# Performance work log

Measured on AMD Instinct MI355X. Metric: run time of the kernel, lower is better.

Reference implementation:

```python
import jax, jax.numpy as jnp
import numpy as np

MOMENTUM = 0.9
BN_EPS = 1e-5
NORM_EPS = 1e-12
NUM_CLASSES = 10000
DIM_MLP = 512
NUM_EXPERTS = 3
FEAT_DIM = 256
N = 4096


def _l2norm(x, axis=-1):
    # F.normalize: x / max(||x||, eps)
    n = jnp.sqrt(jnp.sum(x * x, axis=axis, keepdims=True))
    return x / jnp.maximum(n, NORM_EPS)


def setup_inputs() -> dict:
    key = jax.random.key(0)
    ks = jax.random.split(key, 8)
    feat_in = jax.random.normal(ks[0], (N, DIM_MLP * NUM_EXPERTS), dtype=jnp.float32)
    label = jax.random.randint(ks[1], (N,), 0, NUM_CLASSES, dtype=jnp.int32)
    # encoder params
    W1 = jax.random.normal(ks[2], (DIM_MLP * NUM_EXPERTS, DIM_MLP), dtype=jnp.float32) / np.sqrt(DIM_MLP * NUM_EXPERTS)
    b1 = jnp.zeros((DIM_MLP,), dtype=jnp.float32)
    gamma = jnp.ones((DIM_MLP,), dtype=jnp.float32)
    beta = jnp.zeros((DIM_MLP,), dtype=jnp.float32)
    W2 = jax.random.normal(ks[3], (DIM_MLP, FEAT_DIM), dtype=jnp.float32) / np.sqrt(DIM_MLP)
    b2 = jnp.zeros((FEAT_DIM,), dtype=jnp.float32)
    # memory bank buffer: randn then row-normalized (as in __init__)
    memory_pt = _l2norm(jax.random.normal(ks[4], (NUM_CLASSES, FEAT_DIM), dtype=jnp.float32))
    return {"feat_in": feat_in, "label": label, "W1": W1, "b1": b1,
            "gamma": gamma, "beta": beta, "W2": W2, "b2": b2,
            "memory_pt": memory_pt}


def _encoder(feat_in, W1, b1, gamma, beta, W2, b2):
    h = feat_in @ W1 + b1                       # [N, dim_mlp]
    # BatchNorm1d in training mode: batch statistics (biased variance)
    mu = jnp.mean(h, axis=0)
    var = jnp.mean((h - mu) ** 2, axis=0)
    h = (h - mu) * jax.lax.rsqrt(var + BN_EPS) * gamma + beta
    h = jax.nn.relu(h)
    out = h @ W2 + b2                           # [N, 256]
    return _l2norm(out, axis=1)


def _update_memory(memory_pt, feat, label):
    # Strictly sequential per-sample momentum update (order matters for
    # duplicate labels), each touched row renormalized — lax.scan recurrence.
    def step(mem, xy):
        x, y = xy
        pt = MOMENTUM * mem[y] + (1.0 - MOMENTUM) * x
        pt = _l2norm(pt, axis=0)
        return mem.at[y].set(pt), None
    mem, _ = jax.lax.scan(step, memory_pt, (feat, label))
    return mem


def reference(feat_in, label, W1, b1, gamma, beta, W2, b2, memory_pt):
    feat = _encoder(feat_in, W1, b1, gamma, beta, W2, b2)   # [N, 256], unit rows
    # memory_pt.detach(): no grad flows through the memory bank
    mem = _update_memory(jax.lax.stop_gradient(memory_pt),
                         jax.lax.stop_gradient(feat), label)
    mem = jax.lax.stop_gradient(mem)
    sim_logit = jnp.einsum('nc,kc->nk', feat, mem)          # [N, K]
    return sim_logit
```

## Files before the change

kernel.cpp:

```cpp
#include <hip/hip_runtime.h>
#include <stdint.h>

typedef _Float16 f16;
typedef _Float16 f16x2 __attribute__((ext_vector_type(2)));
typedef _Float16 f16x4 __attribute__((ext_vector_type(4)));
typedef _Float16 f16x8 __attribute__((ext_vector_type(8)));
typedef float f32x4 __attribute__((ext_vector_type(4)));

typedef __attribute__((address_space(1))) void gvoid;
typedef __attribute__((address_space(3))) void lvoid;

#define NROWS 4096
#define DIMIN 1536
#define DMLP 512
#define FDIM 256
#define NCLS 10000
#define NPAD 10112

__device__ __forceinline__ void load_lds16(const void* g, void* l) {
    __builtin_amdgcn_global_load_lds((gvoid*)g, (lvoid*)l, 16, 0, 0);
}

template<int TM, int TN>
__global__ __launch_bounds__(256) void gemm_t(
    const f16* __restrict__ A, const f16* __restrict__ Bt,
    float* __restrict__ C, const float* __restrict__ bias,
    int K, int ldc, int Nstore)
{
    constexpr int BK = 64;
    constexpr int AM = TM / 32;
    constexpr int AN = TN / 32;
    constexpr int CA = TM * 8;
    constexpr int CB = TN * 8;
    constexpr int RTOT = (CA + CB) / 256;

    __shared__ f16 As[TM * BK];
    __shared__ f16 Bs[TN * BK];

    const int tid  = threadIdx.x;
    const int lane = tid & 63;
    const int w    = tid >> 6;
    const int wm   = (w >> 1) * (TM / 2);
    const int wn   = (w & 1) * (TN / 2);
    const int row0 = blockIdx.x * TM;
    const int col0 = blockIdx.y * TN;
    const int quad = lane >> 4;
    const int r16  = lane & 15;

    f32x4 acc[AM][AN] = {};

    const f16* gsrc[RTOT];
    f16* ldst[RTOT];
#pragma unroll
    for (int r = 0; r < RTOT; ++r) {
        int c = tid + r * 256;
        bool isA = (c < CA);
        int cc = isA ? c : c - CA;
        int row = cc >> 3;
        int gs = (cc & 7) ^ (row & 7);
        gsrc[r] = (isA ? A + (size_t)(row0 + row) * K
                       : Bt + (size_t)(col0 + row) * K) + gs * 8;
        ldst[r] = (isA ? As : Bs) + cc * 8;
    }

    for (int k0 = 0; k0 < K; k0 += BK) {
#pragma unroll
        for (int r = 0; r < RTOT; ++r)
            load_lds16(gsrc[r] + k0, ldst[r]);
        __syncthreads();

#pragma unroll
        for (int ks = 0; ks < 2; ++ks) {
            f16x8 af[AM], bq[AN];
#pragma unroll
            for (int mi = 0; mi < AM; ++mi) {
                int row = wm + mi * 16 + r16;
                int slot = (ks * 4 + quad) ^ (r16 & 7);
                af[mi] = *(const f16x8*)&As[row * BK + slot * 8];
            }
#pragma unroll
            for (int ni = 0; ni < AN; ++ni) {
                int row = wn + ni * 16 + r16;
                int slot = (ks * 4 + quad) ^ (r16 & 7);
                bq[ni] = *(const f16x8*)&Bs[row * BK + slot * 8];
            }
#pragma unroll
            for (int mi = 0; mi < AM; ++mi)
#pragma unroll
                for (int ni = 0; ni < AN; ++ni)
                    acc[mi][ni] = __builtin_amdgcn_mfma_f32_16x16x32_f16(
                        af[mi], bq[ni], acc[mi][ni], 0, 0, 0);
        }
        __syncthreads();
    }

#pragma unroll
    for (int mi = 0; mi < AM; ++mi) {
#pragma unroll
        for (int ni = 0; ni < AN; ++ni) {
            int col = col0 + wn + ni * 16 + r16;
            if (col < Nstore) {
                float bv = bias ? bias[col] : 0.0f;
                int rowb = row0 + wm + mi * 16 + quad * 4;
#pragma unroll
                for (int r = 0; r < 4; ++r)
                    C[(size_t)(rowb + r) * ldc + col] = acc[mi][ni][r] + bv;
            }
        }
    }
}

__global__ void zero_k(float* __restrict__ p, int n) {
    int i = blockIdx.x * 256 + threadIdx.x;
    if (i < n) p[i] = 0.0f;
}

__global__ void f32_to_f16_k(const float* __restrict__ in, f16* __restrict__ out, int n4) {
    int i = blockIdx.x * 256 + threadIdx.x;
    if (i >= n4) return;
    float4 v = *(const float4*)&in[(size_t)i * 4];
    f16x4 o = {(f16)v.x, (f16)v.y, (f16)v.z, (f16)v.w};
    *(f16x4*)&out[(size_t)i * 4] = o;
}

__global__ void transpose_to_f16_k(const float* __restrict__ in, f16* __restrict__ out, int R, int C) {
    int idx = blockIdx.x * 256 + threadIdx.x;
    if (idx >= R * C) return;
    int n = idx / R, k = idx - n * R;
    out[idx] = (f16)in[(size_t)k * C + n];
}

__global__ void bn_stats_k(const float* __restrict__ h, float* __restrict__ sums, float* __restrict__ sqs) {
    int t = threadIdx.x, b = blockIdx.x;
    int c = t * 2;
    float s0 = 0.f, s1 = 0.f, q0 = 0.f, q1 = 0.f;
    for (int r = b; r < NROWS; r += 128) {
        float2 v = *(const float2*)&h[(size_t)r * DMLP + c];
        s0 += v.x; s1 += v.y; q0 += v.x * v.x; q1 += v.y * v.y;
    }
    atomicAdd(&sums[c], s0);
    atomicAdd(&sums[c + 1], s1);
    atomicAdd(&sqs[c], q0);
    atomicAdd(&sqs[c + 1], q1);
}

__global__ void bn_finish_k(const float* __restrict__ sums, const float* __restrict__ sqs,
                            const float* __restrict__ gamma, const float* __restrict__ beta,
                            float* __restrict__ scale, float* __restrict__ shift) {
    int c = blockIdx.x * 256 + threadIdx.x;
    if (c >= DMLP) return;
    const float inv_n = 1.0f / 4096.0f;
    float mu = sums[c] * inv_n;
    float var = fmaxf(sqs[c] * inv_n - mu * mu, 0.0f);
    float a = rsqrtf(var + 1e-5f) * gamma[c];
    scale[c] = a;
    shift[c] = beta[c] - mu * a;
}

__global__ void bn_apply_k(const float* __restrict__ h, const float* __restrict__ scale,
                           const float* __restrict__ shift, f16* __restrict__ out) {
    int i = blockIdx.x * 256 + threadIdx.x;
    int c = (i & 127) * 4;
    float4 v = *(const float4*)&h[(size_t)i * 4];
    float4 sc = *(const float4*)&scale[c];
    float4 sh = *(const float4*)&shift[c];
    f16x4 o = {(f16)fmaxf(v.x * sc.x + sh.x, 0.0f),
               (f16)fmaxf(v.y * sc.y + sh.y, 0.0f),
               (f16)fmaxf(v.z * sc.z + sh.z, 0.0f),
               (f16)fmaxf(v.w * sc.w + sh.w, 0.0f)};
    *(f16x4*)&out[(size_t)i * 4] = o;
}

__global__ void l2norm_k(const float* __restrict__ X, float* __restrict__ Y, f16* __restrict__ Yh) {
    int wv = (blockIdx.x * 256 + threadIdx.x) >> 6;
    int lane = threadIdx.x & 63;
    float4 v = *(const float4*)&X[(size_t)wv * FDIM + lane * 4];
    float s = v.x * v.x + v.y * v.y + v.z * v.z + v.w * v.w;
#pragma unroll
    for (int off = 32; off > 0; off >>= 1) s += __shfl_xor(s, off);
    float inv = 1.0f / fmaxf(sqrtf(s), 1e-12f);
    float4 o = {v.x * inv, v.y * inv, v.z * inv, v.w * inv};
    *(float4*)&Y[(size_t)wv * FDIM + lane * 4] = o;
    f16x4 oh = {(f16)o.x, (f16)o.y, (f16)o.z, (f16)o.w};
    *(f16x4*)&Yh[(size_t)wv * FDIM + lane * 4] = oh;
}

__global__ void chain_k(const int* __restrict__ label, const float* __restrict__ feat,
                        const float* __restrict__ mp, f16* __restrict__ memh) {
    int y = (blockIdx.x * 256 + threadIdx.x) >> 6;
    int lane = threadIdx.x & 63;
    float4 m = {0.f, 0.f, 0.f, 0.f};
    if (y < NCLS) {
        m = *(const float4*)&mp[(size_t)y * FDIM + lane * 4];
        for (int g = 0; g < 64; ++g) {
            int lab = label[g * 64 + lane];
            unsigned long long mask = __ballot(lab == y);
            while (mask) {
                int b = __builtin_ctzll(mask);
                mask &= mask - 1;
                int i = g * 64 + b;
                float4 x = *(const float4*)&feat[(size_t)i * FDIM + lane * 4];
                m.x = 0.9f * m.x + 0.1f * x.x;
                m.y = 0.9f * m.y + 0.1f * x.y;
                m.z = 0.9f * m.z + 0.1f * x.z;
                m.w = 0.9f * m.w + 0.1f * x.w;
                float s = m.x * m.x + m.y * m.y + m.z * m.z + m.w * m.w;
#pragma unroll
                for (int off = 32; off > 0; off >>= 1) s += __shfl_xor(s, off);
                float inv = 1.0f / fmaxf(sqrtf(s), 1e-12f);
                m.x *= inv; m.y *= inv; m.z *= inv; m.w *= inv;
            }
        }
    }
    f16x4 o = {(f16)m.x, (f16)m.y, (f16)m.z, (f16)m.w};
    *(f16x4*)&memh[(size_t)y * FDIM + lane * 4] = o;
}

extern "C" void kernel_launch(void* const* d_in, const int* in_sizes, int n_in,
                              void* d_out, int out_size, void* d_ws, size_t ws_size,
                              hipStream_t stream) {
    const float* feat_in = (const float*)d_in[0];
    const int*   label   = (const int*)d_in[1];
    const float* W1      = (const float*)d_in[2];
    const float* b1      = (const float*)d_in[3];
    const float* gamma   = (const float*)d_in[4];
    const float* beta    = (const float*)d_in[5];
    const float* W2      = (const float*)d_in[6];
    const float* b2      = (const float*)d_in[7];
    const float* mp      = (const float*)d_in[8];
    float* out = (float*)d_out;

    char* w = (char*)d_ws;
    f16* A1h   = (f16*)w;   w += (size_t)NROWS * DIMIN * 2;
    f16* W1t   = (f16*)w;   w += (size_t)DMLP * DIMIN * 2;
    f16* W2t   = (f16*)w;   w += (size_t)FDIM * DMLP * 2;
    float* h   = (float*)w; w += (size_t)NROWS * DMLP * 4;
    f16* h2    = (f16*)w;   w += (size_t)NROWS * DMLP * 2;
    float* out2= (float*)w; w += (size_t)NROWS * FDIM * 4;
    float* feat= (float*)w; w += (size_t)NROWS * FDIM * 4;
    f16* feath = (f16*)w;   w += (size_t)NROWS * FDIM * 2;
    f16* memh  = (f16*)w;   w += (size_t)NPAD * FDIM * 2;
    float* sums= (float*)w; w += DMLP * 4;
    float* sqs = (float*)w; w += DMLP * 4;
    float* bnsc= (float*)w; w += DMLP * 4;
    float* bnsh= (float*)w; w += DMLP * 4;

    zero_k<<<4, 256, 0, stream>>>(sums, 2 * DMLP);
    f32_to_f16_k<<<(NROWS * DIMIN / 4) / 256, 256, 0, stream>>>(feat_in, A1h, NROWS * DIMIN / 4);
    transpose_to_f16_k<<<(DIMIN * DMLP) / 256, 256, 0, stream>>>(W1, W1t, DIMIN, DMLP);
    transpose_to_f16_k<<<(DMLP * FDIM) / 256, 256, 0, stream>>>(W2, W2t, DMLP, FDIM);

    {
        dim3 g(NROWS / 64, DMLP / 64);
        gemm_t<64, 64><<<g, 256, 0, stream>>>(A1h, W1t, h, b1, DIMIN, DMLP, DMLP);
    }

    bn_stats_k<<<128, 256, 0, stream>>>(h, sums, sqs);
    bn_finish_k<<<2, 256, 0, stream>>>(sums, sqs, gamma, beta, bnsc, bnsh);
    bn_apply_k<<<(NROWS * DMLP / 4) / 256, 256, 0, stream>>>(h, bnsc, bnsh, h2);

    {
        dim3 g(NROWS / 64, FDIM / 64);
        gemm_t<64, 64><<<g, 256, 0, stream>>>(h2, W2t, out2, b2, DMLP, FDIM, FDIM);
    }

    l2norm_k<<<NROWS / 4, 256, 0, stream>>>(out2, feat, feath);

    chain_k<<<NPAD / 4, 256, 0, stream>>>(label, feat, mp, memh);

    {
        dim3 g(NROWS / 128, NPAD / 128);
        gemm_t<128, 128><<<g, 256, 0, stream>>>(feath, memh, out, nullptr, FDIM, NCLS, NCLS);
    }
}
```

Baseline: 322.8 us.

## Fuse prep kernels, BN finish into apply, L2 norm into second GEMM, retile final GEMM

Merges the zeroing, fp16 conversion and both weight transposes into one prep launch. Folds the BN finish step into the apply kernel. Adds a dedicated second GEMM with full-row tiles (32x256) that applies the bias and L2 normalization in its epilogue, which removes the intermediate buffer and the separate norm kernel. Changes the final similarity GEMM tile from 128x128 to 256x128. These cut launch count and intermediate memory traffic, at the cost of recomputing BN stats per thread and fewer blocks in the fused and retiled GEMMs.

```diff
diff --git a/kernel.cpp b/kernel.cpp
--- a/kernel.cpp
+++ b/kernel.cpp
@@ -71,19 +71,14 @@
 
 #pragma unroll
         for (int ks = 0; ks < 2; ++ks) {
+            const int slot = (ks * 4 + quad) ^ (r16 & 7);
             f16x8 af[AM], bq[AN];
 #pragma unroll
-            for (int mi = 0; mi < AM; ++mi) {
-                int row = wm + mi * 16 + r16;
-                int slot = (ks * 4 + quad) ^ (r16 & 7);
-                af[mi] = *(const f16x8*)&As[row * BK + slot * 8];
-            }
-#pragma unroll
-            for (int ni = 0; ni < AN; ++ni) {
-                int row = wn + ni * 16 + r16;
-                int slot = (ks * 4 + quad) ^ (r16 & 7);
-                bq[ni] = *(const f16x8*)&Bs[row * BK + slot * 8];
-            }
+            for (int mi = 0; mi < AM; ++mi)
+                af[mi] = *(const f16x8*)&As[(wm + mi * 16 + r16) * BK + slot * 8];
+#pragma unroll
+            for (int ni = 0; ni < AN; ++ni)
+                bq[ni] = *(const f16x8*)&Bs[(wn + ni * 16 + r16) * BK + slot * 8];
 #pragma unroll
             for (int mi = 0; mi < AM; ++mi)
 #pragma unroll
@@ -110,24 +105,127 @@
     }
 }
 
-__global__ void zero_k(float* __restrict__ p, int n) {
-    int i = blockIdx.x * 256 + threadIdx.x;
-    if (i < n) p[i] = 0.0f;
-}
-
-__global__ void f32_to_f16_k(const float* __restrict__ in, f16* __restrict__ out, int n4) {
-    int i = blockIdx.x * 256 + threadIdx.x;
-    if (i >= n4) return;
-    float4 v = *(const float4*)&in[(size_t)i * 4];
-    f16x4 o = {(f16)v.x, (f16)v.y, (f16)v.z, (f16)v.w};
-    *(f16x4*)&out[(size_t)i * 4] = o;
-}
-
-__global__ void transpose_to_f16_k(const float* __restrict__ in, f16* __restrict__ out, int R, int C) {
+__global__ __launch_bounds__(256) void gemm2_l2_k(
+    const f16* __restrict__ A, const f16* __restrict__ Bt,
+    const float* __restrict__ bias,
+    float* __restrict__ feat, f16* __restrict__ feath)
+{
+    constexpr int TM = 32, TN = 256, BK = 64, K = 512;
+    constexpr int AN = 8;
+    constexpr int CA = TM * 8;
+    constexpr int CB = TN * 8;
+    constexpr int RTOT = (CA + CB) / 256;
+
+    __shared__ f16 As[TM * BK];
+    __shared__ f16 Bs[TN * BK];
+    __shared__ float part[2][TM];
+
+    const int tid = threadIdx.x, lane = tid & 63, w = tid >> 6;
+    const int wm = (w >> 1) * 16;
+    const int wh = (w & 1);
+    const int wn = wh * 128;
+    const int row0 = blockIdx.x * TM;
+    const int quad = lane >> 4, r16 = lane & 15;
+
+    f32x4 acc[AN] = {};
+
+    const f16* gsrc[RTOT];
+    f16* ldst[RTOT];
+#pragma unroll
+    for (int r = 0; r < RTOT; ++r) {
+        int c = tid + r * 256;
+        bool isA = (c < CA);
+        int cc = isA ? c : c - CA;
+        int row = cc >> 3;
+        int gs = (cc & 7) ^ (row & 7);
+        gsrc[r] = (isA ? A + (size_t)(row0 + row) * K
+                       : Bt + (size_t)row * K) + gs * 8;
+        ldst[r] = (isA ? As : Bs) + cc * 8;
+    }
+
+    for (int k0 = 0; k0 < K; k0 += BK) {
+#pragma unroll
+        for (int r = 0; r < RTOT; ++r)
+            load_lds16(gsrc[r] + k0, ldst[r]);
+        __syncthreads();
+#pragma unroll
+        for (int ks = 0; ks < 2; ++ks) {
+            const int slot = (ks * 4 + quad) ^ (r16 & 7);
+            f16x8 af = *(const f16x8*)&As[(wm + r16) * BK + slot * 8];
+#pragma unroll
+            for (int ni = 0; ni < AN; ++ni) {
+                f16x8 bq = *(const f16x8*)&Bs[(wn + ni * 16 + r16) * BK + slot * 8];
+                acc[ni] = __builtin_amdgcn_mfma_f32_16x16x32_f16(af, bq, acc[ni], 0, 0, 0);
+            }
+        }
+        __syncthreads();
+    }
+
+    float s[4] = {0.f, 0.f, 0.f, 0.f};
+#pragma unroll
+    for (int ni = 0; ni < AN; ++ni) {
+        float b = bias[wn + ni * 16 + r16];
+#pragma unroll
+        for (int r = 0; r < 4; ++r) {
+            acc[ni][r] += b;
+            s[r] += acc[ni][r] * acc[ni][r];
+        }
+    }
+#pragma unroll
+    for (int off = 1; off < 16; off <<= 1)
+#pragma unroll
+        for (int r = 0; r < 4; ++r)
+            s[r] += __shfl_xor(s[r], off);
+    if (r16 == 0)
+#pragma unroll
+        for (int r = 0; r < 4; ++r)
+            part[wh][wm + quad * 4 + r] = s[r];
+    __syncthreads();
+
+    float inv[4];
+#pragma unroll
+    for (int r = 0; r < 4; ++r) {
+        int row = wm + quad * 4 + r;
+        float tot = part[0][row] + part[1][row];
+        inv[r] = 1.0f / fmaxf(sqrtf(tot), 1e-12f);
+    }
+#pragma unroll
+    for (int ni = 0; ni < AN; ++ni) {
+        int col = wn + ni * 16 + r16;
+#pragma unroll
+        for (int r = 0; r < 4; ++r) {
+            int row = row0 + wm + quad * 4 + r;
+            float v = acc[ni][r] * inv[r];
+            feat[(size_t)row * FDIM + col] = v;
+            feath[(size_t)row * FDIM + col] = (f16)v;
+        }
+    }
+}
+
+__global__ void prep_k(const float* __restrict__ feat_in, const float* __restrict__ W1,
+                       const float* __restrict__ W2, f16* __restrict__ A1h,
+                       f16* __restrict__ W1t, f16* __restrict__ W2t,
+                       float* __restrict__ stats) {
     int idx = blockIdx.x * 256 + threadIdx.x;
-    if (idx >= R * C) return;
-    int n = idx / R, k = idx - n * R;
-    out[idx] = (f16)in[(size_t)k * C + n];
+    if (idx < 1024) { stats[idx] = 0.0f; return; }
+    idx -= 1024;
+    if (idx < NROWS * DIMIN / 4) {
+        float4 v = *(const float4*)&feat_in[(size_t)idx * 4];
+        f16x4 o = {(f16)v.x, (f16)v.y, (f16)v.z, (f16)v.w};
+        *(f16x4*)&A1h[(size_t)idx * 4] = o;
+        return;
+    }
+    idx -= NROWS * DIMIN / 4;
+    if (idx < DMLP * DIMIN) {
+        int n = idx / DIMIN, k = idx - n * DIMIN;
+        W1t[idx] = (f16)W1[(size_t)k * DMLP + n];
+        return;
+    }
+    idx -= DMLP * DIMIN;
+    if (idx < FDIM * DMLP) {
+        int n = idx / DMLP, k = idx - n * DMLP;
+        W2t[idx] = (f16)W2[(size_t)k * FDIM + n];
+    }
 }
 
 __global__ void bn_stats_k(const float* __restrict__ h, float* __restrict__ sums, float* __restrict__ sqs) {
@@ -144,45 +242,28 @@
     atomicAdd(&sqs[c + 1], q1);
 }
 
-__global__ void bn_finish_k(const float* __restrict__ sums, const float* __restrict__ sqs,
-                            const float* __restrict__ gamma, const float* __restrict__ beta,
-                            float* __restrict__ scale, float* __restrict__ shift) {
-    int c = blockIdx.x * 256 + threadIdx.x;
-    if (c >= DMLP) return;
-    const float inv_n = 1.0f / 4096.0f;
-    float mu = sums[c] * inv_n;
-    float var = fmaxf(sqs[c] * inv_n - mu * mu, 0.0f);
-    float a = rsqrtf(var + 1e-5f) * gamma[c];
-    scale[c] = a;
-    shift[c] = beta[c] - mu * a;
-}
-
-__global__ void bn_apply_k(const float* __restrict__ h, const float* __restrict__ scale,
-                           const float* __restrict__ shift, f16* __restrict__ out) {
+__global__ void bn_apply_k(const float* __restrict__ h, const float* __restrict__ sums,
+                           const float* __restrict__ sqs, const float* __restrict__ gamma,
+                           const float* __restrict__ beta, f16* __restrict__ out) {
     int i = blockIdx.x * 256 + threadIdx.x;
     int c = (i & 127) * 4;
-    float4 v = *(const float4*)&h[(size_t)i * 4];
-    float4 sc = *(const float4*)&scale[c];
-    float4 sh = *(const float4*)&shift[c];
-    f16x4 o = {(f16)fmaxf(v.x * sc.x + sh.x, 0.0f),
-               (f16)fmaxf(v.y * sc.y + sh.y, 0.0f),
-               (f16)fmaxf(v.z * sc.z + sh.z, 0.0f),
-               (f16)fmaxf(v.w * sc.w + sh.w, 0.0f)};
+    float4 v  = *(const float4*)&h[(size_t)i * 4];
+    float4 sm = *(const float4*)&sums[c];
+    float4 sq = *(const float4*)&sqs[c];
+    float4 gm = *(const float4*)&gamma[c];
+    float4 bt = *(const float4*)&beta[c];
+    const float inv_n = 1.0f / 4096.0f;
+    float mu, var, a;
+    mu = sm.x * inv_n; var = fmaxf(sq.x * inv_n - mu * mu, 0.f); a = rsqrtf(var + 1e-5f) * gm.x;
+    float o0 = fmaxf((v.x - mu) * a + bt.x, 0.f);
+    mu = sm.y * inv_n; var = fmaxf(sq.y * inv_n - mu * mu, 0.f); a = rsqrtf(var + 1e-5f) * gm.y;
+    float o1 = fmaxf((v.y - mu) * a + bt.y, 0.f);
+    mu = sm.z * inv_n; var = fmaxf(sq.z * inv_n - mu * mu, 0.f); a = rsqrtf(var + 1e-5f) * gm.z;
+    float o2 = fmaxf((v.z - mu) * a + bt.z, 0.f);
+    mu = sm.w * inv_n; var = fmaxf(sq.w * inv_n - mu * mu, 0.f); a = rsqrtf(var + 1e-5f) * gm.w;
+    float o3 = fmaxf((v.w - mu) * a + bt.w, 0.f);
+    f16x4 o = {(f16)o0, (f16)o1, (f16)o2, (f16)o3};
     *(f16x4*)&out[(size_t)i * 4] = o;
-}
-
-__global__ void l2norm_k(const float* __restrict__ X, float* __restrict__ Y, f16* __restrict__ Yh) {
-    int wv = (blockIdx.x * 256 + threadIdx.x) >> 6;
-    int lane = threadIdx.x & 63;
-    float4 v = *(const float4*)&X[(size_t)wv * FDIM + lane * 4];
-    float s = v.x * v.x + v.y * v.y + v.z * v.z + v.w * v.w;
-#pragma unroll
-    for (int off = 32; off > 0; off >>= 1) s += __shfl_xor(s, off);
-    float inv = 1.0f / fmaxf(sqrtf(s), 1e-12f);
-    float4 o = {v.x * inv, v.y * inv, v.z * inv, v.w * inv};
-    *(float4*)&Y[(size_t)wv * FDIM + lane * 4] = o;
-    f16x4 oh = {(f16)o.x, (f16)o.y, (f16)o.z, (f16)o.w};
-    *(f16x4*)&Yh[(size_t)wv * FDIM + lane * 4] = oh;
 }
 
 __global__ void chain_k(const int* __restrict__ label, const float* __restrict__ feat,
@@ -236,19 +317,14 @@
     f16* W2t   = (f16*)w;   w += (size_t)FDIM * DMLP * 2;
     float* h   = (float*)w; w += (size_t)NROWS * DMLP * 4;
     f16* h2    = (f16*)w;   w += (size_t)NROWS * DMLP * 2;
-    float* out2= (float*)w; w += (size_t)NROWS * FDIM * 4;
     float* feat= (float*)w; w += (size_t)NROWS * FDIM * 4;
     f16* feath = (f16*)w;   w += (size_t)NROWS * FDIM * 2;
     f16* memh  = (f16*)w;   w += (size_t)NPAD * FDIM * 2;
     float* sums= (float*)w; w += DMLP * 4;
     float* sqs = (float*)w; w += DMLP * 4;
-    float* bnsc= (float*)w; w += DMLP * 4;
-    float* bnsh= (float*)w; w += DMLP * 4;
-
-    zero_k<<<4, 256, 0, stream>>>(sums, 2 * DMLP);
-    f32_to_f16_k<<<(NROWS * DIMIN / 4) / 256, 256, 0, stream>>>(feat_in, A1h, NROWS * DIMIN / 4);
-    transpose_to_f16_k<<<(DIMIN * DMLP) / 256, 256, 0, stream>>>(W1, W1t, DIMIN, DMLP);
-    transpose_to_f16_k<<<(DMLP * FDIM) / 256, 256, 0, stream>>>(W2, W2t, DMLP, FDIM);
+
+    prep_k<<<(1024 + NROWS * DIMIN / 4 + DMLP * DIMIN + FDIM * DMLP) / 256, 256, 0, stream>>>(
+        feat_in, W1, W2, A1h, W1t, W2t, sums);
 
     {
         dim3 g(NROWS / 64, DMLP / 64);
@@ -256,20 +332,15 @@
     }
 
     bn_stats_k<<<128, 256, 0, stream>>>(h, sums, sqs);
-    bn_finish_k<<<2, 256, 0, stream>>>(sums, sqs, gamma, beta, bnsc, bnsh);
-    bn_apply_k<<<(NROWS * DMLP / 4) / 256, 256, 0, stream>>>(h, bnsc, bnsh, h2);
+
+    bn_apply_k<<<(NROWS * DMLP / 4) / 256, 256, 0, stream>>>(h, sums, sqs, gamma, beta, h2);
+
+    gemm2_l2_k<<<NROWS / 32, 256, 0, stream>>>(h2, W2t, b2, feat, feath);
+
+    chain_k<<<NPAD / 4, 256, 0, stream>>>(label, feat, mp, memh);
 
     {
-        dim3 g(NROWS / 64, FDIM / 64);
-        gemm_t<64, 64><<<g, 256, 0, stream>>>(h2, W2t, out2, b2, DMLP, FDIM, FDIM);
-    }
-
-    l2norm_k<<<NROWS / 4, 256, 0, stream>>>(out2, feat, feath);
-
-    chain_k<<<NPAD / 4, 256, 0, stream>>>(label, feat, mp, memh);
-
-    {
-        dim3 g(NROWS / 128, NPAD / 128);
-        gemm_t<128, 128><<<g, 256, 0, stream>>>(feath, memh, out, nullptr, FDIM, NCLS, NCLS);
-    }
-}
+        dim3 g(NROWS / 256, NPAD / 128);
+        gemm_t<256, 128><<<g, 256, 0, stream>>>(feath, memh, out, nullptr, FDIM, NCLS, NCLS);
+    }
+}
```

New measurement: 329.6 us. 1.02x slower.
